# Optimization experiments

Measured on AMD Instinct MI355X. Metric: run time of the kernel, lower is better.

## Reference

```python
import jax, jax.numpy as jnp
import numpy as np

N_NODES = 100000
N_EDGES = 1600000
IN_DIM, HID_DIM, OUT_DIM = 128, 32, 32
NEG_SLOPE = 0.2  # DGL GATConv default


def setup_inputs() -> dict:
    key = jax.random.key(0)
    ks = jax.random.split(key, 12)
    features = jax.random.normal(ks[0], (N_NODES, IN_DIM), dtype=jnp.float32)
    src = jax.random.randint(ks[1], (N_EDGES,), 0, N_NODES, dtype=jnp.int32)
    dst = jax.random.randint(ks[2], (N_EDGES,), 0, N_NODES, dtype=jnp.int32)
    s1 = 1.0 / np.sqrt(IN_DIM)
    s2 = 1.0 / np.sqrt(HID_DIM)
    W1 = jax.random.normal(ks[3], (IN_DIM, HID_DIM), dtype=jnp.float32) * s1
    al1 = jax.random.normal(ks[4], (HID_DIM,), dtype=jnp.float32) * s2
    ar1 = jax.random.normal(ks[5], (HID_DIM,), dtype=jnp.float32) * s2
    b1 = jnp.zeros((HID_DIM,), dtype=jnp.float32)
    W2 = jax.random.normal(ks[6], (HID_DIM, OUT_DIM), dtype=jnp.float32) * s2
    al2 = jax.random.normal(ks[7], (OUT_DIM,), dtype=jnp.float32) * s2
    ar2 = jax.random.normal(ks[8], (OUT_DIM,), dtype=jnp.float32) * s2
    b2 = jnp.zeros((OUT_DIM,), dtype=jnp.float32)
    return {"features": features, "src": src, "dst": dst,
            "W1": W1, "al1": al1, "ar1": ar1, "b1": b1,
            "W2": W2, "al2": al2, "ar2": ar2, "b2": b2}


def gat_conv(x, W, a_l, a_r, b, src, dst, n_nodes):
    # x: [N, Din] -> h: [N, D]
    h = x @ W
    el = h @ a_l  # [N] per-node left attention logit
    er = h @ a_r  # [N]
    # per-edge score with LeakyReLU (DGL default negative_slope=0.2)
    e = jax.nn.leaky_relu(el[src] + er[dst], negative_slope=NEG_SLOPE)  # [E]
    # segment softmax over edges grouped by destination node
    emax = jax.ops.segment_max(e, dst, num_segments=n_nodes)  # [N]
    ex = jnp.exp(e - emax[dst])  # [E]
    denom = jax.ops.segment_sum(ex, dst, num_segments=n_nodes)  # [N]
    alpha = ex / denom[dst]  # [E], every edge's dst has degree >= 1
    # scatter-weighted aggregation of source features
    out = jax.ops.segment_sum(h[src] * alpha[:, None], dst, num_segments=n_nodes)
    return out + b


def reference(features, src, dst, W1, al1, ar1, b1, W2, al2, ar2, b2):
    n = features.shape[0]
    h = gat_conv(features, W1, al1, ar1, b1, src, dst, n)
    h = jax.nn.elu(h)
    out = gat_conv(h, W2, al2, ar2, b2, src, dst, n)
    return out  # [N, OUT_DIM]
```

## Files before the change

### kernel.cpp

```cpp
#include <hip/hip_runtime.h>
#include <hip/hip_bf16.h>

#define N_NODES 100000
#define N_EDGES 1600000
#define IN_DIM 128
#define HID 32
#define BW 128
#define NBUCK ((N_NODES + BW - 1) / BW)


using bf16x8 = __attribute__((ext_vector_type(8))) short;
using f32x4  = __attribute__((ext_vector_type(4))) float;

__device__ __forceinline__ short f2bf(float f) {
    return __builtin_bit_cast(short, __float2bfloat16(f));
}
__device__ __forceinline__ float bf2f(short s) {
    return __bfloat162float(__builtin_bit_cast(__hip_bfloat16, s));
}

__global__ __launch_bounds__(256) void gemm1_kernel(
    const float* __restrict__ x, const float* __restrict__ W,
    const float* __restrict__ al, const float* __restrict__ ar,
    __hip_bfloat16* __restrict__ h, float* __restrict__ el, float* __restrict__ er,
    int* __restrict__ bucket_cnt)
{
    __shared__ float Xs[64][132];
    const int tid = threadIdx.x;
    const int row0 = blockIdx.x * 64;

    const int gid = blockIdx.x * 256 + tid;
    if (gid < NBUCK) bucket_cnt[gid] = 0;

    const int lane = tid & 63, wid = tid >> 6;
    const int l15 = lane & 15, g = lane >> 4;

    bf16x8 bh[4][2], bl[4][2];
    #pragma unroll
    for (int q = 0; q < 4; ++q)
        #pragma unroll
        for (int ct = 0; ct < 2; ++ct)
            #pragma unroll
            for (int j = 0; j < 8; ++j) {
                const float wv = W[(32 * q + 8 * g + j) * HID + ct * 16 + l15];
                const short hi = f2bf(wv);
                bh[q][ct][j] = hi;
                bl[q][ct][j] = f2bf(wv - bf2f(hi));
            }

    #pragma unroll
    for (int i = 0; i < 8; ++i) {
        const int f = tid + 256 * i;
        const int r = f >> 5, c4 = f & 31;
        const int gr = row0 + r;
        float4 v = make_float4(0.f, 0.f, 0.f, 0.f);
        if (gr < N_NODES) v = ((const float4*)x)[(size_t)gr * 32 + c4];
        *(float4*)&Xs[r][c4 * 4] = v;
    }
    __syncthreads();

    const int tile = blockIdx.x * 4 + wid;
    if (tile * 16 >= N_NODES) return;
    const int rl = wid * 16 + l15;

    f32x4 acc0 = {0.f, 0.f, 0.f, 0.f}, acc1 = {0.f, 0.f, 0.f, 0.f};
    #pragma unroll
    for (int q = 0; q < 4; ++q) {
        const float4 xa = *(const float4*)&Xs[rl][32 * q + 8 * g];
        const float4 xb = *(const float4*)&Xs[rl][32 * q + 8 * g + 4];
        const float xs[8] = {xa.x, xa.y, xa.z, xa.w, xb.x, xb.y, xb.z, xb.w};
        bf16x8 ah, alo;
        #pragma unroll
        for (int j = 0; j < 8; ++j) {
            const short hi = f2bf(xs[j]);
            ah[j] = hi;
            alo[j] = f2bf(xs[j] - bf2f(hi));
        }
        acc0 = __builtin_amdgcn_mfma_f32_16x16x32_bf16(ah,  bh[q][0], acc0, 0, 0, 0);
        acc0 = __builtin_amdgcn_mfma_f32_16x16x32_bf16(alo, bh[q][0], acc0, 0, 0, 0);
        acc0 = __builtin_amdgcn_mfma_f32_16x16x32_bf16(ah,  bl[q][0], acc0, 0, 0, 0);
        acc1 = __builtin_amdgcn_mfma_f32_16x16x32_bf16(ah,  bh[q][1], acc1, 0, 0, 0);
        acc1 = __builtin_amdgcn_mfma_f32_16x16x32_bf16(alo, bh[q][1], acc1, 0, 0, 0);
        acc1 = __builtin_amdgcn_mfma_f32_16x16x32_bf16(ah,  bl[q][1], acc1, 0, 0, 0);
    }

    const int grow0 = tile * 16 + 4 * g;
    const float a0 = al[l15], a1 = al[16 + l15];
    const float r0 = ar[l15], r1 = ar[16 + l15];
    float pel[4], per_[4];
    #pragma unroll
    for (int i = 0; i < 4; ++i) {
        const int grow = grow0 + i;
        h[(size_t)grow * HID + l15]      = __float2bfloat16(acc0[i]);
        h[(size_t)grow * HID + 16 + l15] = __float2bfloat16(acc1[i]);
        pel[i]  = acc0[i] * a0 + acc1[i] * a1;
        per_[i] = acc0[i] * r0 + acc1[i] * r1;
    }
    #pragma unroll
    for (int m = 1; m < 16; m <<= 1)
        #pragma unroll
        for (int i = 0; i < 4; ++i) {
            pel[i]  += __shfl_xor(pel[i],  m, 16);
            per_[i] += __shfl_xor(per_[i], m, 16);
        }
    if (l15 == 0)
        #pragma unroll
        for (int i = 0; i < 4; ++i) { el[grow0 + i] = pel[i]; er[grow0 + i] = per_[i]; }
}

__global__ __launch_bounds__(256) void bhist_kernel(const int* __restrict__ dst,
                                                    int* __restrict__ bucket_cnt)
{
    __shared__ int hist[NBUCK];
    const int tid = threadIdx.x;
    for (int i = tid; i < NBUCK; i += 256) hist[i] = 0;
    __syncthreads();
    const int t = blockIdx.x * 256 + tid;
    if (t < N_EDGES / 16) {
        const int4* d4 = (const int4*)dst + (size_t)t * 4;
        #pragma unroll
        for (int q = 0; q < 4; ++q) {
            const int4 d = d4[q];
            atomicAdd(&hist[d.x >> 7], 1); atomicAdd(&hist[d.y >> 7], 1);
            atomicAdd(&hist[d.z >> 7], 1); atomicAdd(&hist[d.w >> 7], 1);
        }
    }
    __syncthreads();
    for (int i = tid; i < NBUCK; i += 256) {
        const int hv = hist[i];
        if (hv) atomicAdd(&bucket_cnt[i], hv);
    }
}

__global__ __launch_bounds__(1024) void bscan_kernel(const int* __restrict__ cnt,
                                                     int* __restrict__ base,
                                                     int* __restrict__ gcur)
{
    const int t = threadIdx.x;
    const int v = (t < NBUCK) ? cnt[t] : 0;
    const int lane = t & 63, wid = t >> 6;
    int pre = v;
    #pragma unroll
    for (int off = 1; off < 64; off <<= 1) {
        const int n = __shfl_up(pre, off, 64);
        if (lane >= off) pre += n;
    }
    __shared__ int ws[16];
    if (lane == 63) ws[wid] = pre;
    __syncthreads();
    int wo = 0;
    for (int k = 0; k < wid; ++k) wo += ws[k];
    const int ex = wo + pre - v;
    if (t < NBUCK) { base[t] = ex; gcur[t] = ex; }
}

__global__ __launch_bounds__(256) void bin_kernel(const int* __restrict__ src,
                                                  const int* __restrict__ dst,
                                                  int* __restrict__ gcur,
                                                  int* __restrict__ pairs)
{
    __shared__ int hist[NBUCK];
    __shared__ int cur[NBUCK];
    const int tid = threadIdx.x;
    for (int i = tid; i < NBUCK; i += 256) hist[i] = 0;
    __syncthreads();

    const int t = blockIdx.x * 256 + tid;
    const bool act = t < N_EDGES / 16;
    int4 sv[4], dv[4];
    if (act) {
        const int4* s4 = (const int4*)src + (size_t)t * 4;
        const int4* d4 = (const int4*)dst + (size_t)t * 4;
        #pragma unroll
        for (int q = 0; q < 4; ++q) { sv[q] = s4[q]; dv[q] = d4[q]; }
        #pragma unroll
        for (int q = 0; q < 4; ++q) {
            atomicAdd(&hist[dv[q].x >> 7], 1); atomicAdd(&hist[dv[q].y >> 7], 1);
            atomicAdd(&hist[dv[q].z >> 7], 1); atomicAdd(&hist[dv[q].w >> 7], 1);
        }
    }
    __syncthreads();
    for (int i = tid; i < NBUCK; i += 256) {
        const int hv = hist[i];
        cur[i] = hv ? atomicAdd(&gcur[i], hv) : 0;
    }
    __syncthreads();
    if (act) {
        #pragma unroll
        for (int q = 0; q < 4; ++q) {
            const int ss[4] = {sv[q].x, sv[q].y, sv[q].z, sv[q].w};
            const int dd[4] = {dv[q].x, dv[q].y, dv[q].z, dv[q].w};
            #pragma unroll
            for (int r = 0; r < 4; ++r) {
                const int slot = atomicAdd(&cur[dd[r] >> 7], 1);
                pairs[slot] = (ss[r] << 7) | (dd[r] & (BW - 1));
            }
        }
    }
}

__global__ __launch_bounds__(256) void lsort_kernel(
    const int* __restrict__ bucket_base, const int* __restrict__ bucket_cnt,
    const int* __restrict__ pairs,
    const float* __restrict__ el, const float* __restrict__ er,
    int* __restrict__ deg, int* __restrict__ rowptr,
    int* __restrict__ csr, float* __restrict__ w1)
{
    __shared__ int lhist[BW];
    __shared__ int lcur[BW];
    __shared__ float ers[BW];
    __shared__ int w0tot;
    const int tid = threadIdx.x;
    const int b = blockIdx.x;
    const int node0 = b * BW;
    if (tid < BW) {
        lhist[tid] = 0;
        ers[tid] = (node0 + tid < N_NODES) ? er[node0 + tid] : 0.f;
    }
    __syncthreads();
    const int ebase = bucket_base[b];
    const int ecnt  = bucket_cnt[b];
    for (int i = tid; i < ecnt; i += 256)
        atomicAdd(&lhist[pairs[ebase + i] & (BW - 1)], 1);
    __syncthreads();
    const int lane = tid & 63;
    int v = 0;
    if (tid < BW) v = lhist[tid];
    int pre = v;
    #pragma unroll
    for (int off = 1; off < 64; off <<= 1) {
        const int n = __shfl_up(pre, off, 64);
        if (lane >= off) pre += n;
    }
    if (tid == 63) w0tot = pre;
    __syncthreads();
    if (tid < BW) {
        const int ex = pre - v + (tid >= 64 ? w0tot : 0);
        lcur[tid] = ex;
        const int node = node0 + tid;
        if (node < N_NODES) { deg[node] = v; rowptr[node] = ebase + ex; }
    }
    __syncthreads();
    for (int i = tid; i < ecnt; i += 256) {
        const int p = pairs[ebase + i];
        const int ldst = p & (BW - 1);
        const int slot = atomicAdd(&lcur[ldst], 1);
        csr[ebase + slot] = p;
        float sc = el[p >> 7] + ers[ldst];
        sc = sc > 0.f ? sc : 0.2f * sc;
        w1[ebase + slot] = __expf(sc);
    }
}

__global__ __launch_bounds__(256) void wcalc_kernel(
    const int* __restrict__ bucket_base, const int* __restrict__ bucket_cnt,
    const int* __restrict__ csr,
    const float* __restrict__ el, const float* __restrict__ er,
    float* __restrict__ w)
{
    __shared__ float ers[BW];
    const int tid = threadIdx.x;
    const int b = blockIdx.x;
    const int node0 = b * BW;
    if (tid < BW) ers[tid] = (node0 + tid < N_NODES) ? er[node0 + tid] : 0.f;
    __syncthreads();
    const int ebase = bucket_base[b];
    const int ecnt  = bucket_cnt[b];
    for (int i = tid; i < ecnt; i += 256) {
        const int p = csr[ebase + i];
        float sc = el[p >> 7] + ers[p & (BW - 1)];
        sc = sc > 0.f ? sc : 0.2f * sc;
        w[ebase + i] = __expf(sc);
    }
}

template <int MODE>
__global__ __launch_bounds__(256) void gather_kernel(
    const int* __restrict__ rowptr, const int* __restrict__ deg,
    const int* __restrict__ csr, const float* __restrict__ w,
    const __hip_bfloat16* __restrict__ h, const float* __restrict__ bias,
    float* __restrict__ out)
{
    const int tid = threadIdx.x;
    const int node = blockIdx.x * 8 + (tid >> 5);
    const int col = tid & 31;
    const int cnt = deg[node];
    const int start = rowptr[node];
    float acc = 0.f, den = 0.f;
    int j = 0;
    for (; j + 3 < cnt; j += 4) {
        const int p0 = csr[start + j];
        const int p1 = csr[start + j + 1];
        const int p2 = csr[start + j + 2];
        const int p3 = csr[start + j + 3];
        const float w0 = w[start + j];
        const float w1v = w[start + j + 1];
        const float w2v = w[start + j + 2];
        const float w3v = w[start + j + 3];
        const float h0 = __bfloat162float(h[(size_t)(p0 >> 7) * HID + col]);
        const float h1 = __bfloat162float(h[(size_t)(p1 >> 7) * HID + col]);
        const float h2 = __bfloat162float(h[(size_t)(p2 >> 7) * HID + col]);
        const float h3 = __bfloat162float(h[(size_t)(p3 >> 7) * HID + col]);
        den += (w0 + w1v) + (w2v + w3v);
        acc += w0 * h0 + w1v * h1 + w2v * h2 + w3v * h3;
    }
    for (; j < cnt; ++j) {
        const int p = csr[start + j];
        const float wv = w[start + j];
        den += wv;
        acc += wv * __bfloat162float(h[(size_t)(p >> 7) * HID + col]);
    }
    float v = den > 0.f ? acc / den : 0.f;
    v += bias[col];
    if (MODE == 0) v = v > 0.f ? v : expm1f(v);
    out[(size_t)node * HID + col] = v;
}

__global__ __launch_bounds__(256) void gemm2_kernel(
    const float* __restrict__ x2, const float* __restrict__ W,
    const float* __restrict__ al, const float* __restrict__ ar,
    __hip_bfloat16* __restrict__ h, float* __restrict__ el, float* __restrict__ er)
{
    __shared__ float Ws[HID][36];
    __shared__ float Xs[32][36];
    const int tid = threadIdx.x;
    const int row0 = blockIdx.x * 32;
    {
        const float4 wv = ((const float4*)W)[tid];
        *(float4*)&Ws[tid >> 3][(tid & 7) * 4] = wv;
        const float4 xv = ((const float4*)x2)[(size_t)row0 * 8 + tid];
        *(float4*)&Xs[tid >> 3][(tid & 7) * 4] = xv;
    }
    __syncthreads();

    const int r = tid >> 3, cg = tid & 7;
    const int row = row0 + r;
    float ax = 0.f, ay = 0.f, az = 0.f, aw = 0.f;
    #pragma unroll
    for (int k = 0; k < HID; ++k) {
        const float xv = Xs[r][k];
        const float4 wv = *(const float4*)&Ws[k][cg * 4];
        ax += xv * wv.x; ay += xv * wv.y; az += xv * wv.z; aw += xv * wv.w;
    }

    ushort4 hp;
    hp.x = __builtin_bit_cast(unsigned short, __float2bfloat16(ax));
    hp.y = __builtin_bit_cast(unsigned short, __float2bfloat16(ay));
    hp.z = __builtin_bit_cast(unsigned short, __float2bfloat16(az));
    hp.w = __builtin_bit_cast(unsigned short, __float2bfloat16(aw));
    *(ushort4*)&h[(size_t)row * HID + cg * 4] = hp;

    const int c0 = cg * 4;
    float pel = ax * al[c0] + ay * al[c0 + 1] + az * al[c0 + 2] + aw * al[c0 + 3];
    float per = ax * ar[c0] + ay * ar[c0 + 1] + az * ar[c0 + 2] + aw * ar[c0 + 3];
    #pragma unroll
    for (int m = 1; m < 8; m <<= 1) {
        pel += __shfl_xor(pel, m, 8);
        per += __shfl_xor(per, m, 8);
    }
    if (cg == 0) { el[row] = pel; er[row] = per; }
}

extern "C" void kernel_launch(void* const* d_in, const int* in_sizes, int n_in,
                              void* d_out, int out_size, void* d_ws, size_t ws_size,
                              hipStream_t stream) {
    const float* features = (const float*)d_in[0];
    const int*   src      = (const int*)d_in[1];
    const int*   dst      = (const int*)d_in[2];
    const float* W1       = (const float*)d_in[3];
    const float* al1      = (const float*)d_in[4];
    const float* ar1      = (const float*)d_in[5];
    const float* b1       = (const float*)d_in[6];
    const float* W2       = (const float*)d_in[7];
    const float* al2      = (const float*)d_in[8];
    const float* ar2      = (const float*)d_in[9];
    const float* b2       = (const float*)d_in[10];
    float* out = (float*)d_out;

    int*  bucket_cnt  = (int*)d_ws;
    int*  bucket_base = bucket_cnt + 784;
    int*  gcur        = bucket_base + 784;
    int*  deg         = gcur + 784;
    int*  rowptr      = deg + N_NODES;
    int*  csr         = rowptr + N_NODES;
    int*  pairs       = csr + N_EDGES;
    float* wbuf       = (float*)(pairs + N_EDGES);
    __hip_bfloat16* h = (__hip_bfloat16*)(wbuf + N_EDGES);
    float* el  = (float*)(h + (size_t)N_NODES * HID);
    float* er  = el + N_NODES;
    float* x2  = er + N_NODES;

    const int NB_E16 = (N_EDGES / 16 + 255) / 256;
    const int NB_G1  = (N_NODES + 63) / 64;

    gemm1_kernel<<<NB_G1, 256, 0, stream>>>(features, W1, al1, ar1,
                                            h, el, er, bucket_cnt);
    bhist_kernel<<<NB_E16, 256, 0, stream>>>(dst, bucket_cnt);
    bscan_kernel<<<1, 1024, 0, stream>>>(bucket_cnt, bucket_base, gcur);
    bin_kernel<<<NB_E16, 256, 0, stream>>>(src, dst, gcur, pairs);
    lsort_kernel<<<NBUCK, 256, 0, stream>>>(bucket_base, bucket_cnt, pairs,
                                            el, er, deg, rowptr, csr, wbuf);
    gather_kernel<0><<<N_NODES / 8, 256, 0, stream>>>(rowptr, deg, csr, wbuf,
                                                      h, b1, x2);
    gemm2_kernel<<<N_NODES / 32, 256, 0, stream>>>(x2, W2, al2, ar2, h, el, er);
    wcalc_kernel<<<NBUCK, 256, 0, stream>>>(bucket_base, bucket_cnt, csr,
                                            el, er, wbuf);
    gather_kernel<1><<<N_NODES / 8, 256, 0, stream>>>(rowptr, deg, csr, wbuf,
                                                      h, b2, out);
}
```

Before: 278.9 us.

## Use fixed-capacity buckets, fuse edge weights and gemm2 into gather kernels

Replaces the bucket histogram and scan kernels with fixed-capacity per-bucket regions (CAP slots each), so binning can start right after gemm1. Local sorting now happens in shared memory and writes back in place. The wcalc pass and the stored edge-weight buffer are removed: attention weights are computed on the fly inside the gather via warp shuffles. The layer-2 GEMM and its el/er projections are fused into the first gather's epilogue. Together this cuts kernel launches and global traffic, but it silently truncates any bucket with more than CAP edges, which only holds for roughly uniform random graphs.

```diff
diff --git a/kernel.cpp b/kernel.cpp
--- a/kernel.cpp
+++ b/kernel.cpp
@@ -7,6 +7,7 @@
 #define HID 32
 #define BW 128
 #define NBUCK ((N_NODES + BW - 1) / BW)
+#define CAP 4096
 
 
 using bf16x8 = __attribute__((ext_vector_type(8))) short;
@@ -23,14 +24,14 @@
     const float* __restrict__ x, const float* __restrict__ W,
     const float* __restrict__ al, const float* __restrict__ ar,
     __hip_bfloat16* __restrict__ h, float* __restrict__ el, float* __restrict__ er,
-    int* __restrict__ bucket_cnt)
+    int* __restrict__ gcur)
 {
     __shared__ float Xs[64][132];
     const int tid = threadIdx.x;
     const int row0 = blockIdx.x * 64;
 
     const int gid = blockIdx.x * 256 + tid;
-    if (gid < NBUCK) bucket_cnt[gid] = 0;
+    if (gid < NBUCK) gcur[gid] = gid * CAP;
 
     const int lane = tid & 63, wid = tid >> 6;
     const int l15 = lane & 15, g = lane >> 4;
@@ -106,52 +107,6 @@
     if (l15 == 0)
         #pragma unroll
         for (int i = 0; i < 4; ++i) { el[grow0 + i] = pel[i]; er[grow0 + i] = per_[i]; }
-}
-
-__global__ __launch_bounds__(256) void bhist_kernel(const int* __restrict__ dst,
-                                                    int* __restrict__ bucket_cnt)
-{
-    __shared__ int hist[NBUCK];
-    const int tid = threadIdx.x;
-    for (int i = tid; i < NBUCK; i += 256) hist[i] = 0;
-    __syncthreads();
-    const int t = blockIdx.x * 256 + tid;
-    if (t < N_EDGES / 16) {
-        const int4* d4 = (const int4*)dst + (size_t)t * 4;
-        #pragma unroll
-        for (int q = 0; q < 4; ++q) {
-            const int4 d = d4[q];
-            atomicAdd(&hist[d.x >> 7], 1); atomicAdd(&hist[d.y >> 7], 1);
-            atomicAdd(&hist[d.z >> 7], 1); atomicAdd(&hist[d.w >> 7], 1);
-        }
-    }
-    __syncthreads();
-    for (int i = tid; i < NBUCK; i += 256) {
-        const int hv = hist[i];
-        if (hv) atomicAdd(&bucket_cnt[i], hv);
-    }
-}
-
-__global__ __launch_bounds__(1024) void bscan_kernel(const int* __restrict__ cnt,
-                                                     int* __restrict__ base,
-                                                     int* __restrict__ gcur)
-{
-    const int t = threadIdx.x;
-    const int v = (t < NBUCK) ? cnt[t] : 0;
-    const int lane = t & 63, wid = t >> 6;
-    int pre = v;
-    #pragma unroll
-    for (int off = 1; off < 64; off <<= 1) {
-        const int n = __shfl_up(pre, off, 64);
-        if (lane >= off) pre += n;
-    }
-    __shared__ int ws[16];
-    if (lane == 63) ws[wid] = pre;
-    __syncthreads();
-    int wo = 0;
-    for (int k = 0; k < wid; ++k) wo += ws[k];
-    const int ex = wo + pre - v;
-    if (t < NBUCK) { base[t] = ex; gcur[t] = ex; }
 }
 
 __global__ __launch_bounds__(256) void bin_kernel(const int* __restrict__ src,
@@ -200,28 +155,26 @@
 }
 
 __global__ __launch_bounds__(256) void lsort_kernel(
-    const int* __restrict__ bucket_base, const int* __restrict__ bucket_cnt,
-    const int* __restrict__ pairs,
-    const float* __restrict__ el, const float* __restrict__ er,
-    int* __restrict__ deg, int* __restrict__ rowptr,
-    int* __restrict__ csr, float* __restrict__ w1)
+    const int* __restrict__ gcur, int* __restrict__ pairs,
+    int* __restrict__ deg, int* __restrict__ rowptr)
 {
+    __shared__ int lp[CAP];
+    __shared__ int lc[CAP];
     __shared__ int lhist[BW];
     __shared__ int lcur[BW];
-    __shared__ float ers[BW];
     __shared__ int w0tot;
     const int tid = threadIdx.x;
     const int b = blockIdx.x;
-    const int node0 = b * BW;
-    if (tid < BW) {
-        lhist[tid] = 0;
-        ers[tid] = (node0 + tid < N_NODES) ? er[node0 + tid] : 0.f;
-    }
-    __syncthreads();
-    const int ebase = bucket_base[b];
-    const int ecnt  = bucket_cnt[b];
-    for (int i = tid; i < ecnt; i += 256)
-        atomicAdd(&lhist[pairs[ebase + i] & (BW - 1)], 1);
+    const int rbase = b * CAP;
+    int ecnt = gcur[b] - rbase;
+    if (ecnt > CAP) ecnt = CAP;
+    if (tid < BW) lhist[tid] = 0;
+    __syncthreads();
+    for (int i = tid; i < ecnt; i += 256) {
+        const int p = pairs[rbase + i];
+        lp[i] = p;
+        atomicAdd(&lhist[p & (BW - 1)], 1);
+    }
     __syncthreads();
     const int lane = tid & 63;
     int v = 0;
@@ -237,128 +190,96 @@
     if (tid < BW) {
         const int ex = pre - v + (tid >= 64 ? w0tot : 0);
         lcur[tid] = ex;
-        const int node = node0 + tid;
-        if (node < N_NODES) { deg[node] = v; rowptr[node] = ebase + ex; }
+        const int node = b * BW + tid;
+        if (node < N_NODES) { deg[node] = v; rowptr[node] = rbase + ex; }
     }
     __syncthreads();
     for (int i = tid; i < ecnt; i += 256) {
-        const int p = pairs[ebase + i];
-        const int ldst = p & (BW - 1);
-        const int slot = atomicAdd(&lcur[ldst], 1);
-        csr[ebase + slot] = p;
-        float sc = el[p >> 7] + ers[ldst];
-        sc = sc > 0.f ? sc : 0.2f * sc;
-        w1[ebase + slot] = __expf(sc);
-    }
-}
-
-__global__ __launch_bounds__(256) void wcalc_kernel(
-    const int* __restrict__ bucket_base, const int* __restrict__ bucket_cnt,
-    const int* __restrict__ csr,
-    const float* __restrict__ el, const float* __restrict__ er,
-    float* __restrict__ w)
-{
-    __shared__ float ers[BW];
-    const int tid = threadIdx.x;
-    const int b = blockIdx.x;
-    const int node0 = b * BW;
-    if (tid < BW) ers[tid] = (node0 + tid < N_NODES) ? er[node0 + tid] : 0.f;
-    __syncthreads();
-    const int ebase = bucket_base[b];
-    const int ecnt  = bucket_cnt[b];
-    for (int i = tid; i < ecnt; i += 256) {
-        const int p = csr[ebase + i];
-        float sc = el[p >> 7] + ers[p & (BW - 1)];
-        sc = sc > 0.f ? sc : 0.2f * sc;
-        w[ebase + i] = __expf(sc);
-    }
+        const int p = lp[i];
+        const int slot = atomicAdd(&lcur[p & (BW - 1)], 1);
+        lc[slot] = p;
+    }
+    __syncthreads();
+    for (int i = tid; i < ecnt; i += 256) pairs[rbase + i] = lc[i];
 }
 
 template <int MODE>
 __global__ __launch_bounds__(256) void gather_kernel(
     const int* __restrict__ rowptr, const int* __restrict__ deg,
-    const int* __restrict__ csr, const float* __restrict__ w,
+    const int* __restrict__ csr,
+    const float* __restrict__ el, const float* __restrict__ er,
     const __hip_bfloat16* __restrict__ h, const float* __restrict__ bias,
-    float* __restrict__ out)
+    const float* __restrict__ W2, const float* __restrict__ al2,
+    const float* __restrict__ ar2,
+    __hip_bfloat16* __restrict__ h2, float* __restrict__ el2,
+    float* __restrict__ er2, float* __restrict__ out)
 {
     const int tid = threadIdx.x;
+    float* W2s = nullptr;
+    if constexpr (MODE == 0) {
+        __shared__ float W2s_[HID * HID];
+        W2s = W2s_;
+        ((float4*)W2s)[tid] = ((const float4*)W2)[tid];
+        __syncthreads();
+    }
     const int node = blockIdx.x * 8 + (tid >> 5);
     const int col = tid & 31;
     const int cnt = deg[node];
     const int start = rowptr[node];
-    float acc = 0.f, den = 0.f;
-    int j = 0;
-    for (; j + 3 < cnt; j += 4) {
-        const int p0 = csr[start + j];
-        const int p1 = csr[start + j + 1];
-        const int p2 = csr[start + j + 2];
-        const int p3 = csr[start + j + 3];
-        const float w0 = w[start + j];
-        const float w1v = w[start + j + 1];
-        const float w2v = w[start + j + 2];
-        const float w3v = w[start + j + 3];
-        const float h0 = __bfloat162float(h[(size_t)(p0 >> 7) * HID + col]);
-        const float h1 = __bfloat162float(h[(size_t)(p1 >> 7) * HID + col]);
-        const float h2 = __bfloat162float(h[(size_t)(p2 >> 7) * HID + col]);
-        const float h3 = __bfloat162float(h[(size_t)(p3 >> 7) * HID + col]);
-        den += (w0 + w1v) + (w2v + w3v);
-        acc += w0 * h0 + w1v * h1 + w2v * h2 + w3v * h3;
-    }
-    for (; j < cnt; ++j) {
-        const int p = csr[start + j];
-        const float wv = w[start + j];
-        den += wv;
-        acc += wv * __bfloat162float(h[(size_t)(p >> 7) * HID + col]);
-    }
+    const float erd = er[node];
+    float acc = 0.f, denl = 0.f;
+    for (int base = 0; base < cnt; base += 32) {
+        const int rem = cnt - base;
+        int p = 0; float wv = 0.f;
+        if (col < rem) {
+            p = csr[start + base + col];
+            float sc = el[p >> 7] + erd;
+            sc = sc > 0.f ? sc : 0.2f * sc;
+            wv = __expf(sc);
+        }
+        denl += wv;
+        const int m = rem < 32 ? rem : 32;
+        int k = 0;
+        for (; k + 3 < m; k += 4) {
+            const int   p0 = __shfl(p, k, 32),     p1 = __shfl(p, k + 1, 32);
+            const int   p2 = __shfl(p, k + 2, 32), p3 = __shfl(p, k + 3, 32);
+            const float w0 = __shfl(wv, k, 32),     w1 = __shfl(wv, k + 1, 32);
+            const float w2 = __shfl(wv, k + 2, 32), w3 = __shfl(wv, k + 3, 32);
+            const float h0 = __bfloat162float(h[(size_t)(p0 >> 7) * HID + col]);
+            const float h1 = __bfloat162float(h[(size_t)(p1 >> 7) * HID + col]);
+            const float h2v = __bfloat162float(h[(size_t)(p2 >> 7) * HID + col]);
+            const float h3 = __bfloat162float(h[(size_t)(p3 >> 7) * HID + col]);
+            acc += w0 * h0 + w1 * h1 + w2 * h2v + w3 * h3;
+        }
+        for (; k < m; ++k) {
+            const int pk = __shfl(p, k, 32);
+            const float wk = __shfl(wv, k, 32);
+            acc += wk * __bfloat162float(h[(size_t)(pk >> 7) * HID + col]);
+        }
+    }
+    float den = denl;
+    #pragma unroll
+    for (int mm = 16; mm > 0; mm >>= 1) den += __shfl_xor(den, mm, 32);
+
     float v = den > 0.f ? acc / den : 0.f;
     v += bias[col];
-    if (MODE == 0) v = v > 0.f ? v : expm1f(v);
-    out[(size_t)node * HID + col] = v;
-}
-
-__global__ __launch_bounds__(256) void gemm2_kernel(
-    const float* __restrict__ x2, const float* __restrict__ W,
-    const float* __restrict__ al, const float* __restrict__ ar,
-    __hip_bfloat16* __restrict__ h, float* __restrict__ el, float* __restrict__ er)
-{
-    __shared__ float Ws[HID][36];
-    __shared__ float Xs[32][36];
-    const int tid = threadIdx.x;
-    const int row0 = blockIdx.x * 32;
-    {
-        const float4 wv = ((const float4*)W)[tid];
-        *(float4*)&Ws[tid >> 3][(tid & 7) * 4] = wv;
-        const float4 xv = ((const float4*)x2)[(size_t)row0 * 8 + tid];
-        *(float4*)&Xs[tid >> 3][(tid & 7) * 4] = xv;
-    }
-    __syncthreads();
-
-    const int r = tid >> 3, cg = tid & 7;
-    const int row = row0 + r;
-    float ax = 0.f, ay = 0.f, az = 0.f, aw = 0.f;
-    #pragma unroll
-    for (int k = 0; k < HID; ++k) {
-        const float xv = Xs[r][k];
-        const float4 wv = *(const float4*)&Ws[k][cg * 4];
-        ax += xv * wv.x; ay += xv * wv.y; az += xv * wv.z; aw += xv * wv.w;
-    }
-
-    ushort4 hp;
-    hp.x = __builtin_bit_cast(unsigned short, __float2bfloat16(ax));
-    hp.y = __builtin_bit_cast(unsigned short, __float2bfloat16(ay));
-    hp.z = __builtin_bit_cast(unsigned short, __float2bfloat16(az));
-    hp.w = __builtin_bit_cast(unsigned short, __float2bfloat16(aw));
-    *(ushort4*)&h[(size_t)row * HID + cg * 4] = hp;
-
-    const int c0 = cg * 4;
-    float pel = ax * al[c0] + ay * al[c0 + 1] + az * al[c0 + 2] + aw * al[c0 + 3];
-    float per = ax * ar[c0] + ay * ar[c0 + 1] + az * ar[c0 + 2] + aw * ar[c0 + 3];
-    #pragma unroll
-    for (int m = 1; m < 8; m <<= 1) {
-        pel += __shfl_xor(pel, m, 8);
-        per += __shfl_xor(per, m, 8);
-    }
-    if (cg == 0) { el[row] = pel; er[row] = per; }
+    if constexpr (MODE == 0) {
+        v = v > 0.f ? v : expm1f(v);
+        float hacc = 0.f;
+        #pragma unroll
+        for (int k = 0; k < HID; ++k)
+            hacc += __shfl(v, k, 32) * W2s[k * HID + col];
+        h2[(size_t)node * HID + col] = __float2bfloat16(hacc);
+        float pel = hacc * al2[col], per = hacc * ar2[col];
+        #pragma unroll
+        for (int mm = 16; mm > 0; mm >>= 1) {
+            pel += __shfl_xor(pel, mm, 32);
+            per += __shfl_xor(per, mm, 32);
+        }
+        if (col == 0) { el2[node] = pel; er2[node] = per; }
+    } else {
+        out[(size_t)node * HID + col] = v;
+    }
 }
 
 extern "C" void kernel_launch(void* const* d_in, const int* in_sizes, int n_in,
@@ -377,34 +298,30 @@
     const float* b2       = (const float*)d_in[10];
     float* out = (float*)d_out;
 
-    int*  bucket_cnt  = (int*)d_ws;
-    int*  bucket_base = bucket_cnt + 784;
-    int*  gcur        = bucket_base + 784;
-    int*  deg         = gcur + 784;
-    int*  rowptr      = deg + N_NODES;
-    int*  csr         = rowptr + N_NODES;
-    int*  pairs       = csr + N_EDGES;
-    float* wbuf       = (float*)(pairs + N_EDGES);
-    __hip_bfloat16* h = (__hip_bfloat16*)(wbuf + N_EDGES);
-    float* el  = (float*)(h + (size_t)N_NODES * HID);
-    float* er  = el + N_NODES;
-    float* x2  = er + N_NODES;
+    int*  gcur   = (int*)d_ws;
+    int*  deg    = gcur + 784;
+    int*  rowptr = deg + N_NODES;
+    int*  pairs  = rowptr + N_NODES;
+    __hip_bfloat16* h1 = (__hip_bfloat16*)(pairs + NBUCK * CAP);
+    float* el1 = (float*)(h1 + (size_t)N_NODES * HID);
+    float* er1 = el1 + N_NODES;
+    __hip_bfloat16* h2 = (__hip_bfloat16*)(er1 + N_NODES);
+    float* el2 = (float*)(h2 + (size_t)N_NODES * HID);
+    float* er2 = el2 + N_NODES;
 
     const int NB_E16 = (N_EDGES / 16 + 255) / 256;
     const int NB_G1  = (N_NODES + 63) / 64;
 
     gemm1_kernel<<<NB_G1, 256, 0, stream>>>(features, W1, al1, ar1,
-                                            h, el, er, bucket_cnt);
-    bhist_kernel<<<NB_E16, 256, 0, stream>>>(dst, bucket_cnt);
-    bscan_kernel<<<1, 1024, 0, stream>>>(bucket_cnt, bucket_base, gcur);
+                                            h1, el1, er1, gcur);
     bin_kernel<<<NB_E16, 256, 0, stream>>>(src, dst, gcur, pairs);
-    lsort_kernel<<<NBUCK, 256, 0, stream>>>(bucket_base, bucket_cnt, pairs,
-                                            el, er, deg, rowptr, csr, wbuf);
-    gather_kernel<0><<<N_NODES / 8, 256, 0, stream>>>(rowptr, deg, csr, wbuf,
-                                                      h, b1, x2);
-    gemm2_kernel<<<N_NODES / 32, 256, 0, stream>>>(x2, W2, al2, ar2, h, el, er);
-    wcalc_kernel<<<NBUCK, 256, 0, stream>>>(bucket_base, bucket_cnt, csr,
-                                            el, er, wbuf);
-    gather_kernel<1><<<N_NODES / 8, 256, 0, stream>>>(rowptr, deg, csr, wbuf,
-                                                      h, b2, out);
-}
+    lsort_kernel<<<NBUCK, 256, 0, stream>>>(gcur, pairs, deg, rowptr);
+    gather_kernel<0><<<N_NODES / 8, 256, 0, stream>>>(rowptr, deg, pairs,
+                                                      el1, er1, h1, b1,
+                                                      W2, al2, ar2,
+                                                      h2, el2, er2, nullptr);
+    gather_kernel<1><<<N_NODES / 8, 256, 0, stream>>>(rowptr, deg, pairs,
+                                                      el2, er2, h2, b2,
+                                                      nullptr, nullptr, nullptr,
+                                                      nullptr, nullptr, nullptr, out);
+}
```

After: 237.9 us. -14.7%, faster.
